# Kernel optimization log

Hardware: AMD Instinct MI355X
Metric: run time of the kernel (lower is better)

## Reference

```python
import jax, jax.numpy as jnp
import numpy as np

D = 8        # q_ndim (= dof_ndim)
HID = 200    # hidden_size
N = 16384    # batch of states
EPS = 0.1    # qdot regularizer coefficient in L()


def _lagrangian(z, Ws, bs):
    # z: (2D,) = [q, qdot]; angular_dims=() so CosSin is an identity pass-through
    v = z[D:]
    h = z
    for W, b in zip(Ws[:-1], bs[:-1]):
        h = jax.nn.softplus(h @ W + b)   # FCsoftplus blocks
    L = (h @ Ws[-1] + bs[-1])[0]          # final Linear -> scalar (Reshape(-1))
    return L + EPS * jnp.dot(v, v)


def setup_inputs():
    key = jax.random.key(0)
    ks = jax.random.split(key, 5)
    z = jax.random.normal(ks[0], (N, 2 * D), dtype=jnp.float32)
    t = jnp.zeros((), dtype=jnp.float32)

    def lin(k, fi, fo, scale):
        return (jax.random.normal(k, (fi, fo), dtype=jnp.float32)
                * jnp.float32(scale / np.sqrt(fi)))

    W0 = lin(ks[1], 2 * D, HID, 1.0)
    W1 = lin(ks[2], HID, HID, 1.0)
    W2 = lin(ks[3], HID, HID, 1.0)
    W3 = lin(ks[4], HID, 1, 0.01)  # small head keeps mass matrix M well conditioned
    b0 = jnp.zeros((HID,), jnp.float32)  # zero_bias init per FCsoftplus/Linear
    b1 = jnp.zeros((HID,), jnp.float32)
    b2 = jnp.zeros((HID,), jnp.float32)
    b3 = jnp.zeros((1,), jnp.float32)
    return dict(t=t, z=z, W0=W0, b0=b0, W1=W1, b1=b1, W2=W2, b2=b2, W3=W3, b3=b3)


def reference(t, z, W0, b0, W1, b1, W2, b2, W3, b3):
    # Euler-Lagrange dynamics (LagrangianDynamics):
    #   M a = dL/dq - (d2L/dq dv) v,  M = d2L/dv2;  dz/dt = [v, a]
    Ws = (W0, W1, W2, W3)
    bs = (b0, b1, b2, b3)
    Lfn = lambda zz: _lagrangian(zz, Ws, bs)

    def dyn_single(zi):
        g = jax.grad(Lfn)(zi)              # (2D,)  = [dL/dq, dL/dv]
        H = jax.jacfwd(jax.grad(Lfn))(zi)  # (2D,2D) Hessian of L wrt z
        v = zi[D:]
        M = H[D:, D:]                      # d(dL/dv)/dv  -> mass matrix
        C = H[D:, :D]                      # d(dL/dv)/dq
        F = g[:D] - C @ v
        a = jnp.linalg.solve(M, F)
        return jnp.concatenate([v, a])     # (2D,)

    return jax.vmap(dyn_single)(z)         # (N, 2D)
```

## Files before the change

kernel.cpp:

```cpp
#include <hip/hip_runtime.h>
#include <math.h>

#define DD 8
#define ZD 16
#define HID 200
#define EPSL 0.1f
#define BS 16
#define NTHREADS 1024
#define NKC 7
#define NMT 13
#define XSTR 216
#define CSTR 212
#define HSTR 20
#define WSTR 208
#define NTAN 8
#define NT4 4

#define KSC 1024.0f
#define SSC 64.0f
#define INV_K (1.0f/1024.0f)
#define INV_KS (1.0f/65536.0f)

typedef _Float16 half8 __attribute__((ext_vector_type(8)));
typedef _Float16 half4v __attribute__((ext_vector_type(4)));
typedef _Float16 half2v __attribute__((ext_vector_type(2)));
typedef __fp16 fp16x2 __attribute__((ext_vector_type(2)));
typedef float float4v __attribute__((ext_vector_type(4)));

#define S4 (NKC*NMT*64*8)
#define OFF_W1T 0
#define OFF_W2T (S4)
#define OFF_W1  (2*S4)
#define OFF_W2  (3*S4)
#define OFF_W0T (4*S4)
#define OFF_W0  (4*S4 + NMT*64*8)
#define WS_HALFS (4*S4 + NMT*64*8 + NKC*64*8)

__global__ void prep(const float* __restrict__ W0, const float* __restrict__ W1,
                     const float* __restrict__ W2, _Float16* __restrict__ ws)
{
    int idx = blockIdx.x * 256 + threadIdx.x;
    if (idx >= WS_HALFS) return;
    float v = 0.f;
    if (idx < 4*S4) {
        int arr = idx / S4, e = idx % S4;
        int kc = e / (NMT*64*8); int r = e % (NMT*64*8);
        int mt = r / (64*8); r %= 64*8;
        int lane = r / 8, j = r % 8;
        int m = mt*16 + (lane & 15);
        int k = kc*32 + (lane >> 4)*8 + j;
        if (m < HID && k < HID) {
            if      (arr == 0) v = W1[k*HID + m];
            else if (arr == 1) v = W2[k*HID + m];
            else if (arr == 2) v = W1[m*HID + k];
            else               v = W2[m*HID + k];
        }
    } else if (idx < OFF_W0) {
        int e = idx - OFF_W0T;
        int mt = e / (64*8); int r = e % (64*8);
        int lane = r / 8, j = r % 8;
        int m = mt*16 + (lane & 15);
        int k = (lane >> 4)*8 + j;
        if (m < HID && k < ZD) v = W0[k*HID + m];
    } else {
        int e = idx - OFF_W0;
        int kc = e / (64*8); int r = e % (64*8);
        int lane = r / 8, j = r % 8;
        int m = (lane & 15);
        int k = kc*32 + (lane >> 4)*8 + j;
        if (k < HID) v = W0[m*HID + k];
    }
    ws[idx] = (_Float16)v;
}

__device__ __forceinline__ half4v pk4(float4v a) {
    half2v lo = __builtin_bit_cast(half2v, __builtin_amdgcn_cvt_pkrtz(a.x, a.y));
    half2v hi = __builtin_bit_cast(half2v, __builtin_amdgcn_cvt_pkrtz(a.z, a.w));
    return __builtin_shufflevector(lo, hi, 0, 1, 2, 3);
}
__device__ __forceinline__ void sig_sp(float x, float& sp, float& sg) {
    float e = __expf(-fabsf(x));
    float r = 1.0f / (1.0f + e);
    sg = (x >= 0.f) ? r : (1.0f - r);
    sp = fmaxf(x, 0.f) + __logf(1.f + e);
}

template<int NTILES>
__device__ __forceinline__ void run_mv(const half8* __restrict__ Asw,
                                       const _Float16* __restrict__ Xsrc,
                                       int mt0, int mtc, int lane,
                                       float4v acc[2][NTILES])
{
    const int lm = lane & 15, q = lane >> 4;
#pragma unroll
    for (int m = 0; m < 2; ++m)
#pragma unroll
        for (int n = 0; n < NTILES; ++n)
            acc[m][n] = (float4v){0.f, 0.f, 0.f, 0.f};
    for (int kc = 0; kc < NKC; ++kc) {
        half8 a[2];
#pragma unroll
        for (int m = 0; m < 2; ++m)
            if (m < mtc) a[m] = Asw[(kc*NMT + mt0 + m)*64 + lane];
        half8 x[NTILES];
#pragma unroll
        for (int n = 0; n < NTILES; ++n)
            x[n] = *(const half8*)(Xsrc + (n*16 + lm)*XSTR + kc*32 + q*8);
#pragma unroll
        for (int m = 0; m < 2; ++m)
            if (m < mtc)
#pragma unroll
                for (int n = 0; n < NTILES; ++n)
                    acc[m][n] = __builtin_amdgcn_mfma_f32_16x16x32_f16(a[m], x[n], acc[m][n], 0, 0, 0);
    }
}

__global__ void __launch_bounds__(NTHREADS, 4)
lnn_main(const float* __restrict__ z,
         const float* __restrict__ W0, const float* __restrict__ b0,
         const float* __restrict__ b1, const float* __restrict__ b2,
         const float* __restrict__ W3,
         const _Float16* __restrict__ ws,
         float* __restrict__ out)
{
    __shared__ alignas(16) _Float16 Xt[128*XSTR];
    __shared__ alignas(16) _Float16 Xb[128*XSTR];
    __shared__ alignas(16) _Float16 Cf[5][16*CSTR];
    __shared__ alignas(16) _Float16 Xz[16*40];
    __shared__ alignas(16) _Float16 bsh[4*WSTR];
    __shared__ alignas(16) _Float16 w0t[NTAN*WSTR];
    __shared__ alignas(16) float gsh[16*HSTR];
    __shared__ alignas(16) float Hr[128*HSTR];

    const int tid  = threadIdx.x;
    const int wave = tid >> 6;
    const int lane = tid & 63;
    const int lm   = lane & 15;
    const int q    = lane >> 4;
    const int s0   = blockIdx.x * BS;

    const int twm  = wave >> 1;
    const int twn  = wave & 1;
    const int mt0t = (twm < 5) ? twm*2 : (twm + 5);
    const int mtct = (twm < 5) ? 2 : 1;

    const half8* W1Tsw = (const half8*)(ws + OFF_W1T);
    const half8* W2Tsw = (const half8*)(ws + OFF_W2T);
    const half8* W1sw  = (const half8*)(ws + OFF_W1);
    const half8* W2sw  = (const half8*)(ws + OFF_W2);
    const half8* W0Tsw = (const half8*)(ws + OFF_W0T);
    const half8* W0sw  = (const half8*)(ws + OFF_W0);

    if (tid < 256) {
        int s = tid >> 4, k = tid & 15;
        Xz[s*40 + k]      = (_Float16)z[(s0 + s)*ZD + k];
        Xz[s*40 + 16 + k] = (_Float16)0.f;
    }
    for (int idx = tid; idx < 128*16; idx += NTHREADS) {
        int r = idx >> 4, c = 200 + (idx & 15);
        Xt[r*XSTR + c] = (_Float16)0.f;
        Xb[r*XSTR + c] = (_Float16)0.f;
    }
    for (int idx = tid; idx < 4*WSTR; idx += NTHREADS) {
        int l = idx / WSTR, u = idx % WSTR;
        float v = 0.f;
        if (u < HID) {
            if      (l == 0) v = b0[u];
            else if (l == 1) v = b1[u];
            else if (l == 2) v = b2[u];
            else             v = KSC * W3[u];
        }
        bsh[idx] = (_Float16)v;
    }
    for (int idx = tid; idx < NTAN*WSTR; idx += NTHREADS) {
        int t = idx / WSTR, u = idx % WSTR;
        w0t[idx] = (_Float16)((u < HID) ? SSC * W0[(DD + t)*HID + u] : 0.f);
    }
    __syncthreads();

    float4v acc1[2][1];
    const int ubf = wave*16 + q*4;

    if (wave < NMT) {
        acc1[0][0] = (float4v){0.f,0.f,0.f,0.f};
        half8 xz = *(const half8*)(Xz + lm*40 + q*8);
        half8 a = W0Tsw[wave*64 + lane];
        acc1[0][0] = __builtin_amdgcn_mfma_f32_16x16x32_f16(a, xz, acc1[0][0], 0, 0, 0);
        half4v bb = *(const half4v*)(&bsh[0*WSTR + ubf]);
        float h[4], p[4];
#pragma unroll
        for (int r = 0; r < 4; ++r) {
            float av = acc1[0][0][r] + (float)bb[r];
            sig_sp(av, h[r], p[r]);
        }
        *(half4v*)(&Xt[lm*XSTR + ubf])     = pk4((float4v){h[0],h[1],h[2],h[3]});
        *(half4v*)(&Cf[0][lm*CSTR + ubf])  = pk4((float4v){p[0],p[1],p[2],p[3]});
    }
    __syncthreads();

    if (wave < NMT) run_mv<1>(W1Tsw, Xt, wave, 1, lane, acc1);
    __syncthreads();
    if (wave < NMT) {
        half4v bb = *(const half4v*)(&bsh[1*WSTR + ubf]);
        float h[4], p[4];
#pragma unroll
        for (int r = 0; r < 4; ++r) {
            float av = acc1[0][0][r] + (float)bb[r];
            sig_sp(av, h[r], p[r]);
        }
        *(half4v*)(&Xt[lm*XSTR + ubf])    = pk4((float4v){h[0],h[1],h[2],h[3]});
        *(half4v*)(&Cf[1][lm*CSTR + ubf]) = pk4((float4v){p[0],p[1],p[2],p[3]});
    }
    __syncthreads();

    if (wave < NMT) run_mv<1>(W2Tsw, Xt, wave, 1, lane, acc1);
    __syncthreads();
    if (wave < NMT) {
        half4v bb = *(const half4v*)(&bsh[2*WSTR + ubf]);
        half4v w3 = *(const half4v*)(&bsh[3*WSTR + ubf]);
        float d2[4], c2[4];
#pragma unroll
        for (int r = 0; r < 4; ++r) {
            float av = acc1[0][0][r] + (float)bb[r];
            float e = __expf(-fabsf(av));
            float rr = 1.f / (1.f + e);
            float sg = (av >= 0.f) ? rr : (1.f - rr);
            float wk = (float)w3[r];
            d2[r] = wk * sg;
            c2[r] = wk * sg * (1.f - sg);
        }
        *(half4v*)(&Xt[lm*XSTR + ubf])    = pk4((float4v){d2[0],d2[1],d2[2],d2[3]});
        *(half4v*)(&Cf[2][lm*CSTR + ubf]) = pk4((float4v){c2[0],c2[1],c2[2],c2[3]});
    }
    __syncthreads();

    if (wave < NMT) run_mv<1>(W2sw, Xt, wave, 1, lane, acc1);
    __syncthreads();
    if (wave < NMT) {
        half4v p1 = *(const half4v*)(&Cf[1][lm*CSTR + ubf]);
        half4v u1 = pk4(acc1[0][0]);
        half4v one = {(_Float16)1.f,(_Float16)1.f,(_Float16)1.f,(_Float16)1.f};
        *(half4v*)(&Xt[lm*XSTR + ubf])    = u1 * p1;
        *(half4v*)(&Cf[3][lm*CSTR + ubf]) = u1 * (one - p1);
    }
    __syncthreads();

    if (wave < NMT) run_mv<1>(W1sw, Xt, wave, 1, lane, acc1);
    __syncthreads();
    if (wave < NMT) {
        half4v p0 = *(const half4v*)(&Cf[0][lm*CSTR + ubf]);
        half4v u0 = pk4(acc1[0][0]);
        half4v one = {(_Float16)1.f,(_Float16)1.f,(_Float16)1.f,(_Float16)1.f};
        half4v d0 = u0 * p0;
        *(half4v*)(&Xt[lm*XSTR + ubf])    = d0;
        *(half4v*)(&Cf[4][lm*CSTR + ubf]) = d0 * (one - p0);
    }
    __syncthreads();

    if (wave == 0) {
        float4v g = (float4v){0.f,0.f,0.f,0.f};
        for (int kc = 0; kc < NKC; ++kc) {
            half8 a = W0sw[kc*64 + lane];
            half8 x = *(const half8*)(Xt + lm*XSTR + kc*32 + q*8);
            g = __builtin_amdgcn_mfma_f32_16x16x32_f16(a, x, g, 0, 0, 0);
        }
        float4v gv; gv.x = g.x*INV_K; gv.y = g.y*INV_K; gv.z = g.z*INV_K; gv.w = g.w*INV_K;
        *(float4v*)(&gsh[lm*HSTR + q*4]) = gv;
    } else {
        for (int idx = tid - 64; idx < 128*50; idx += NTHREADS - 64) {
            int row = idx / 50, u = (idx % 50)*4;
            int s = row & 15, t = row >> 4;
            half4v p0 = *(const half4v*)(&Cf[0][s*CSTR + u]);
            half4v w0 = *(const half4v*)(&w0t[t*WSTR + u]);
            *(half4v*)(&Xb[row*XSTR + u]) = p0 * w0;
        }
    }
    __syncthreads();

    float4v acc4[2][NT4];

    run_mv<NT4>(W1Tsw, Xb + twn*64*XSTR, mt0t, mtct, lane, acc4);
    __syncthreads();
#pragma unroll
    for (int m = 0; m < 2; ++m)
        if (m < mtct) {
            const int ub = (mt0t + m)*16 + q*4;
            half4v p1 = *(const half4v*)(&Cf[1][lm*CSTR + ub]);
#pragma unroll
            for (int n = 0; n < NT4; ++n) {
                int row = (twn*NT4 + n)*16 + lm;
                *(half4v*)(&Xt[row*XSTR + ub]) = pk4(acc4[m][n]) * p1;
            }
        }
    __syncthreads();

    run_mv<NT4>(W2Tsw, Xt + twn*64*XSTR, mt0t, mtct, lane, acc4);
    __syncthreads();
#pragma unroll
    for (int m = 0; m < 2; ++m)
        if (m < mtct) {
            const int ub = (mt0t + m)*16 + q*4;
            half4v c2 = *(const half4v*)(&Cf[2][lm*CSTR + ub]);
#pragma unroll
            for (int n = 0; n < NT4; ++n) {
                int row = (twn*NT4 + n)*16 + lm;
                *(half4v*)(&Xb[row*XSTR + ub]) = pk4(acc4[m][n]) * c2;
            }
        }
    __syncthreads();

    run_mv<NT4>(W2sw, Xb + twn*64*XSTR, mt0t, mtct, lane, acc4);
    __syncthreads();
#pragma unroll
    for (int m = 0; m < 2; ++m)
        if (m < mtct) {
            const int ub = (mt0t + m)*16 + q*4;
            half4v p1 = *(const half4v*)(&Cf[1][lm*CSTR + ub]);
            half4v c3 = *(const half4v*)(&Cf[3][lm*CSTR + ub]);
#pragma unroll
            for (int n = 0; n < NT4; ++n) {
                int row = (twn*NT4 + n)*16 + lm;
                half4v th1 = *(const half4v*)(&Xt[row*XSTR + ub]);
                *(half4v*)(&Xb[row*XSTR + ub]) = pk4(acc4[m][n]) * p1 + c3 * th1;
            }
        }
    __syncthreads();

    run_mv<NT4>(W1sw, Xb + twn*64*XSTR, mt0t, mtct, lane, acc4);
    __syncthreads();
#pragma unroll
    for (int m = 0; m < 2; ++m)
        if (m < mtct) {
            const int ub = (mt0t + m)*16 + q*4;
            half4v p0 = *(const half4v*)(&Cf[0][lm*CSTR + ub]);
            half4v c4 = *(const half4v*)(&Cf[4][lm*CSTR + ub]);
#pragma unroll
            for (int n = 0; n < NT4; ++n) {
                int row = (twn*NT4 + n)*16 + lm;
                half4v w0 = *(const half4v*)(&w0t[(twn*NT4 + n)*WSTR + ub]);
                *(half4v*)(&Xt[row*XSTR + ub]) = pk4(acc4[m][n]) * p0 + c4 * w0;
            }
        }
    __syncthreads();

    if (wave < 8) {
        float4v hacc = (float4v){0.f,0.f,0.f,0.f};
        for (int kc = 0; kc < NKC; ++kc) {
            half8 a = W0sw[kc*64 + lane];
            half8 x = *(const half8*)(Xt + (wave*16 + lm)*XSTR + kc*32 + q*8);
            hacc = __builtin_amdgcn_mfma_f32_16x16x32_f16(a, x, hacc, 0, 0, 0);
        }
        int row = wave*16 + lm;
        float4v hv;
        hv.x = hacc.x*INV_KS; hv.y = hacc.y*INV_KS;
        hv.z = hacc.z*INV_KS; hv.w = hacc.w*INV_KS;
        *(float4v*)(&Hr[row*HSTR + q*4]) = hv;
    }
    __syncthreads();

    if (tid < BS) {
        const int s = tid;
        float M[DD][DD], F[DD], v[DD], a[DD];
#pragma unroll
        for (int c = 0; c < DD; ++c) v[c] = z[(s0 + s)*ZD + DD + c];
#pragma unroll
        for (int r = 0; r < DD; ++r) {
            float f = gsh[s*HSTR + r];
#pragma unroll
            for (int c = 0; c < DD; ++c) {
                M[r][c] = Hr[(r*16 + s)*HSTR + DD + c] + ((r == c) ? 2.f*EPSL : 0.f);
                f -= Hr[(r*16 + s)*HSTR + c] * v[c];
            }
            F[r] = f;
        }
#pragma unroll
        for (int col = 0; col < DD; ++col) {
            const float inv = 1.f / M[col][col];
#pragma unroll
            for (int r = col + 1; r < DD; ++r) {
                const float fac = M[r][col] * inv;
#pragma unroll
                for (int c = col + 1; c < DD; ++c) M[r][c] -= fac * M[col][c];
                F[r] -= fac * F[col];
            }
        }
#pragma unroll
        for (int r = DD - 1; r >= 0; --r) {
            float ssum = F[r];
#pragma unroll
            for (int c = r + 1; c < DD; ++c) ssum -= M[r][c] * a[c];
            a[r] = ssum / M[r][r];
        }
        float* op = out + (size_t)(s0 + s)*ZD;
#pragma unroll
        for (int c = 0; c < DD; ++c) { op[c] = v[c]; op[DD + c] = a[c]; }
    }
}

extern "C" void kernel_launch(void* const* d_in, const int* in_sizes, int n_in,
                              void* d_out, int out_size, void* d_ws, size_t ws_size,
                              hipStream_t stream)
{
    const float* z  = (const float*)d_in[1];
    const float* W0 = (const float*)d_in[2];
    const float* b0 = (const float*)d_in[3];
    const float* W1 = (const float*)d_in[4];
    const float* b1 = (const float*)d_in[5];
    const float* W2 = (const float*)d_in[6];
    const float* b2 = (const float*)d_in[7];
    const float* W3 = (const float*)d_in[8];
    float* out = (float*)d_out;
    _Float16* ws = (_Float16*)d_ws;

    const int n = in_sizes[1] / (2*DD);

    prep<<<dim3((WS_HALFS + 255)/256), dim3(256), 0, stream>>>(W0, W1, W2, ws);
    lnn_main<<<dim3(n / BS), dim3(NTHREADS), 0, stream>>>(
        z, W0, b0, b1, b2, W3, ws, out);
}
```

Before: 160.1 us.

## Overlap forward/backward matvecs with tangent pass and fuse tangent input construction

Restructures the kernel schedule so the single-row forward and backward matvecs (into a new FB buffer) run in the same barrier phases as the 128-row tangent matmuls. The first tangent matmul now builds its input p0*w0 in registers instead of staging it through shared memory, and the gradient head runs on wave 13 alongside the last tangent step. The aim is fewer __syncthreads phases and less idle time for waves. All shared arrays are packed into one buffer with explicit offsets and padding. The cost is higher register pressure from keeping acc4 and acc1 live together, plus extra zero-padding setup.

```diff
diff --git a/kernel.cpp b/kernel.cpp
--- a/kernel.cpp
+++ b/kernel.cpp
@@ -10,10 +10,9 @@
 #define NKC 7
 #define NMT 13
 #define XSTR 216
-#define CSTR 212
+#define CSTR 216
+#define WSTR 208
 #define HSTR 20
-#define WSTR 208
-#define NTAN 8
 #define NT4 4
 
 #define KSC 1024.0f
@@ -24,7 +23,6 @@
 typedef _Float16 half8 __attribute__((ext_vector_type(8)));
 typedef _Float16 half4v __attribute__((ext_vector_type(4)));
 typedef _Float16 half2v __attribute__((ext_vector_type(2)));
-typedef __fp16 fp16x2 __attribute__((ext_vector_type(2)));
 typedef float float4v __attribute__((ext_vector_type(4)));
 
 #define S4 (NKC*NMT*64*8)
@@ -35,6 +33,17 @@
 #define OFF_W0T (4*S4)
 #define OFF_W0  (4*S4 + NMT*64*8)
 #define WS_HALFS (4*S4 + NMT*64*8 + NKC*64*8)
+
+#define CFSZ  (16*CSTR)
+#define O_XT  0
+#define O_XB  (128*XSTR + 8)
+#define O_CF  (O_XB + 128*XSTR)
+#define O_BSH (O_CF + 5*CFSZ)
+#define O_W0T (O_BSH + 4*WSTR)
+#define O_XZ  (O_W0T + 8*WSTR + 24)
+#define O_GSH (O_XZ + 16*40)
+#define O_HR  (O_GSH + 256)
+#define SMEM_HALFS (O_HR + 128*HSTR*2)
 
 __global__ void prep(const float* __restrict__ W0, const float* __restrict__ W1,
                      const float* __restrict__ W2, _Float16* __restrict__ ws)
@@ -123,14 +132,16 @@
          const _Float16* __restrict__ ws,
          float* __restrict__ out)
 {
-    __shared__ alignas(16) _Float16 Xt[128*XSTR];
-    __shared__ alignas(16) _Float16 Xb[128*XSTR];
-    __shared__ alignas(16) _Float16 Cf[5][16*CSTR];
-    __shared__ alignas(16) _Float16 Xz[16*40];
-    __shared__ alignas(16) _Float16 bsh[4*WSTR];
-    __shared__ alignas(16) _Float16 w0t[NTAN*WSTR];
-    __shared__ alignas(16) float gsh[16*HSTR];
-    __shared__ alignas(16) float Hr[128*HSTR];
+    __shared__ alignas(16) _Float16 smem[SMEM_HALFS];
+    _Float16* const Xt  = smem + O_XT;
+    _Float16* const Xb  = smem + O_XB;
+    _Float16* const Cf  = smem + O_CF;
+    _Float16* const bsh = smem + O_BSH;
+    _Float16* const w0t = smem + O_W0T;
+    _Float16* const Xz  = smem + O_XZ;
+    float*    const gsh = (float*)(smem + O_GSH);
+    float*    const Hr  = (float*)(smem + O_HR);
+    _Float16* const FB  = smem + O_HR;
 
     const int tid  = threadIdx.x;
     const int wave = tid >> 6;
@@ -160,6 +171,18 @@
         int r = idx >> 4, c = 200 + (idx & 15);
         Xt[r*XSTR + c] = (_Float16)0.f;
         Xb[r*XSTR + c] = (_Float16)0.f;
+    }
+    for (int idx = tid; idx < 16*16; idx += NTHREADS) {
+        int r = idx >> 4, c = 200 + (idx & 15);
+        FB[r*XSTR + c] = (_Float16)0.f;
+    }
+    if (tid < 8) {
+        Xt[128*XSTR + tid] = (_Float16)0.f;
+        FB[16*XSTR + tid]  = (_Float16)0.f;
+    }
+    for (int idx = tid; idx < 5*16*8; idx += NTHREADS) {
+        int j = idx >> 7, r = (idx >> 3) & 15, c = 208 + (idx & 7);
+        Cf[j*CFSZ + r*CSTR + c] = (_Float16)0.f;
     }
     for (int idx = tid; idx < 4*WSTR; idx += NTHREADS) {
         int l = idx / WSTR, u = idx % WSTR;
@@ -172,20 +195,21 @@
         }
         bsh[idx] = (_Float16)v;
     }
-    for (int idx = tid; idx < NTAN*WSTR; idx += NTHREADS) {
+    for (int idx = tid; idx < 8*WSTR + 24; idx += NTHREADS) {
         int t = idx / WSTR, u = idx % WSTR;
-        w0t[idx] = (_Float16)((u < HID) ? SSC * W0[(DD + t)*HID + u] : 0.f);
+        w0t[idx] = (_Float16)((t < 8 && u < HID) ? SSC * W0[(DD + t)*HID + u] : 0.f);
     }
     __syncthreads();
 
     float4v acc1[2][1];
+    float4v acc4[2][NT4];
     const int ubf = wave*16 + q*4;
 
     if (wave < NMT) {
         acc1[0][0] = (float4v){0.f,0.f,0.f,0.f};
         half8 xz = *(const half8*)(Xz + lm*40 + q*8);
-        half8 a = W0Tsw[wave*64 + lane];
-        acc1[0][0] = __builtin_amdgcn_mfma_f32_16x16x32_f16(a, xz, acc1[0][0], 0, 0, 0);
+        half8 aw = W0Tsw[wave*64 + lane];
+        acc1[0][0] = __builtin_amdgcn_mfma_f32_16x16x32_f16(aw, xz, acc1[0][0], 0, 0, 0);
         half4v bb = *(const half4v*)(&bsh[0*WSTR + ubf]);
         float h[4], p[4];
 #pragma unroll
@@ -193,12 +217,12 @@
             float av = acc1[0][0][r] + (float)bb[r];
             sig_sp(av, h[r], p[r]);
         }
-        *(half4v*)(&Xt[lm*XSTR + ubf])     = pk4((float4v){h[0],h[1],h[2],h[3]});
-        *(half4v*)(&Cf[0][lm*CSTR + ubf])  = pk4((float4v){p[0],p[1],p[2],p[3]});
-    }
-    __syncthreads();
-
-    if (wave < NMT) run_mv<1>(W1Tsw, Xt, wave, 1, lane, acc1);
+        *(half4v*)(&FB[lm*XSTR + ubf])          = pk4((float4v){h[0],h[1],h[2],h[3]});
+        *(half4v*)(&Cf[0*CFSZ + lm*CSTR + ubf]) = pk4((float4v){p[0],p[1],p[2],p[3]});
+    }
+    __syncthreads();
+
+    if (wave < NMT) run_mv<1>(W1Tsw, FB, wave, 1, lane, acc1);
     __syncthreads();
     if (wave < NMT) {
         half4v bb = *(const half4v*)(&bsh[1*WSTR + ubf]);
@@ -208,13 +232,50 @@
             float av = acc1[0][0][r] + (float)bb[r];
             sig_sp(av, h[r], p[r]);
         }
-        *(half4v*)(&Xt[lm*XSTR + ubf])    = pk4((float4v){h[0],h[1],h[2],h[3]});
-        *(half4v*)(&Cf[1][lm*CSTR + ubf]) = pk4((float4v){p[0],p[1],p[2],p[3]});
-    }
-    __syncthreads();
-
-    if (wave < NMT) run_mv<1>(W2Tsw, Xt, wave, 1, lane, acc1);
-    __syncthreads();
+        *(half4v*)(&FB[lm*XSTR + ubf])          = pk4((float4v){h[0],h[1],h[2],h[3]});
+        *(half4v*)(&Cf[1*CFSZ + lm*CSTR + ubf]) = pk4((float4v){p[0],p[1],p[2],p[3]});
+    }
+    __syncthreads();
+
+    {
+#pragma unroll
+        for (int m = 0; m < 2; ++m)
+#pragma unroll
+            for (int n = 0; n < NT4; ++n)
+                acc4[m][n] = (float4v){0.f, 0.f, 0.f, 0.f};
+        for (int kc = 0; kc < NKC; ++kc) {
+            half8 a[2];
+#pragma unroll
+            for (int m = 0; m < 2; ++m)
+                if (m < mtct) a[m] = W1Tsw[(kc*NMT + mt0t + m)*64 + lane];
+            half8 p0 = *(const half8*)(Cf + 0*CFSZ + lm*CSTR + kc*32 + q*8);
+            half8 x[NT4];
+#pragma unroll
+            for (int n = 0; n < NT4; ++n) {
+                half8 w0 = *(const half8*)(w0t + (twn*NT4 + n)*WSTR + kc*32 + q*8);
+                x[n] = p0 * w0;
+            }
+#pragma unroll
+            for (int m = 0; m < 2; ++m)
+                if (m < mtct)
+#pragma unroll
+                    for (int n = 0; n < NT4; ++n)
+                        acc4[m][n] = __builtin_amdgcn_mfma_f32_16x16x32_f16(a[m], x[n], acc4[m][n], 0, 0, 0);
+        }
+        if (wave < NMT) run_mv<1>(W2Tsw, FB, wave, 1, lane, acc1);
+    }
+    __syncthreads();
+#pragma unroll
+    for (int m = 0; m < 2; ++m)
+        if (m < mtct) {
+            const int ub = (mt0t + m)*16 + q*4;
+            half4v p1 = *(const half4v*)(&Cf[1*CFSZ + lm*CSTR + ub]);
+#pragma unroll
+            for (int n = 0; n < NT4; ++n) {
+                int row = (twn*NT4 + n)*16 + lm;
+                *(half4v*)(&Xt[row*XSTR + ub]) = pk4(acc4[m][n]) * p1;
+            }
+        }
     if (wave < NMT) {
         half4v bb = *(const half4v*)(&bsh[2*WSTR + ubf]);
         half4v w3 = *(const half4v*)(&bsh[3*WSTR + ubf]);
@@ -229,94 +290,43 @@
             d2[r] = wk * sg;
             c2[r] = wk * sg * (1.f - sg);
         }
-        *(half4v*)(&Xt[lm*XSTR + ubf])    = pk4((float4v){d2[0],d2[1],d2[2],d2[3]});
-        *(half4v*)(&Cf[2][lm*CSTR + ubf]) = pk4((float4v){c2[0],c2[1],c2[2],c2[3]});
-    }
-    __syncthreads();
-
-    if (wave < NMT) run_mv<1>(W2sw, Xt, wave, 1, lane, acc1);
-    __syncthreads();
-    if (wave < NMT) {
-        half4v p1 = *(const half4v*)(&Cf[1][lm*CSTR + ubf]);
-        half4v u1 = pk4(acc1[0][0]);
-        half4v one = {(_Float16)1.f,(_Float16)1.f,(_Float16)1.f,(_Float16)1.f};
-        *(half4v*)(&Xt[lm*XSTR + ubf])    = u1 * p1;
-        *(half4v*)(&Cf[3][lm*CSTR + ubf]) = u1 * (one - p1);
-    }
-    __syncthreads();
-
-    if (wave < NMT) run_mv<1>(W1sw, Xt, wave, 1, lane, acc1);
-    __syncthreads();
-    if (wave < NMT) {
-        half4v p0 = *(const half4v*)(&Cf[0][lm*CSTR + ubf]);
-        half4v u0 = pk4(acc1[0][0]);
-        half4v one = {(_Float16)1.f,(_Float16)1.f,(_Float16)1.f,(_Float16)1.f};
-        half4v d0 = u0 * p0;
-        *(half4v*)(&Xt[lm*XSTR + ubf])    = d0;
-        *(half4v*)(&Cf[4][lm*CSTR + ubf]) = d0 * (one - p0);
-    }
-    __syncthreads();
-
-    if (wave == 0) {
-        float4v g = (float4v){0.f,0.f,0.f,0.f};
-        for (int kc = 0; kc < NKC; ++kc) {
-            half8 a = W0sw[kc*64 + lane];
-            half8 x = *(const half8*)(Xt + lm*XSTR + kc*32 + q*8);
-            g = __builtin_amdgcn_mfma_f32_16x16x32_f16(a, x, g, 0, 0, 0);
-        }
-        float4v gv; gv.x = g.x*INV_K; gv.y = g.y*INV_K; gv.z = g.z*INV_K; gv.w = g.w*INV_K;
-        *(float4v*)(&gsh[lm*HSTR + q*4]) = gv;
-    } else {
-        for (int idx = tid - 64; idx < 128*50; idx += NTHREADS - 64) {
-            int row = idx / 50, u = (idx % 50)*4;
-            int s = row & 15, t = row >> 4;
-            half4v p0 = *(const half4v*)(&Cf[0][s*CSTR + u]);
-            half4v w0 = *(const half4v*)(&w0t[t*WSTR + u]);
-            *(half4v*)(&Xb[row*XSTR + u]) = p0 * w0;
-        }
-    }
-    __syncthreads();
-
-    float4v acc4[2][NT4];
-
-    run_mv<NT4>(W1Tsw, Xb + twn*64*XSTR, mt0t, mtct, lane, acc4);
+        *(half4v*)(&FB[lm*XSTR + ubf])          = pk4((float4v){d2[0],d2[1],d2[2],d2[3]});
+        *(half4v*)(&Cf[2*CFSZ + lm*CSTR + ubf]) = pk4((float4v){c2[0],c2[1],c2[2],c2[3]});
+    }
+    __syncthreads();
+
+    run_mv<NT4>(W2Tsw, Xt + twn*64*XSTR, mt0t, mtct, lane, acc4);
+    if (wave < NMT) run_mv<1>(W2sw, FB, wave, 1, lane, acc1);
     __syncthreads();
 #pragma unroll
     for (int m = 0; m < 2; ++m)
         if (m < mtct) {
             const int ub = (mt0t + m)*16 + q*4;
-            half4v p1 = *(const half4v*)(&Cf[1][lm*CSTR + ub]);
+            half4v c2 = *(const half4v*)(&Cf[2*CFSZ + lm*CSTR + ub]);
 #pragma unroll
             for (int n = 0; n < NT4; ++n) {
                 int row = (twn*NT4 + n)*16 + lm;
-                *(half4v*)(&Xt[row*XSTR + ub]) = pk4(acc4[m][n]) * p1;
-            }
-        }
-    __syncthreads();
-
-    run_mv<NT4>(W2Tsw, Xt + twn*64*XSTR, mt0t, mtct, lane, acc4);
+                *(half4v*)(&Xb[row*XSTR + ub]) = pk4(acc4[m][n]) * c2;
+            }
+        }
+    if (wave < NMT) {
+        half4v p1 = *(const half4v*)(&Cf[1*CFSZ + lm*CSTR + ubf]);
+        half4v u1 = pk4(acc1[0][0]);
+        half4v one = {(_Float16)1.f,(_Float16)1.f,(_Float16)1.f,(_Float16)1.f};
+        *(half4v*)(&FB[lm*XSTR + ubf])          = u1 * p1;
+        *(half4v*)(&Cf[3*CFSZ + lm*CSTR + ubf]) = u1 * (one - p1);
+    }
+    __syncthreads();
+
+    run_mv<NT4>(W2sw, Xb + twn*64*XSTR, mt0t, mtct, lane, acc4);
+    if (wave < NMT) run_mv<1>(W1sw, FB, wave, 1, lane, acc1);
     __syncthreads();
 #pragma unroll
     for (int m = 0; m < 2; ++m)
         if (m < mtct) {
             const int ub = (mt0t + m)*16 + q*4;
-            half4v c2 = *(const half4v*)(&Cf[2][lm*CSTR + ub]);
-#pragma unroll
-            for (int n = 0; n < NT4; ++n) {
-                int row = (twn*NT4 + n)*16 + lm;
-                *(half4v*)(&Xb[row*XSTR + ub]) = pk4(acc4[m][n]) * c2;
-            }
-        }
-    __syncthreads();
-
-    run_mv<NT4>(W2sw, Xb + twn*64*XSTR, mt0t, mtct, lane, acc4);
-    __syncthreads();
-#pragma unroll
-    for (int m = 0; m < 2; ++m)
-        if (m < mtct) {
-            const int ub = (mt0t + m)*16 + q*4;
-            half4v p1 = *(const half4v*)(&Cf[1][lm*CSTR + ub]);
-            half4v c3 = *(const half4v*)(&Cf[3][lm*CSTR + ub]);
+            half4v p1 = *(const half4v*)(&Cf[1*CFSZ + lm*CSTR + ub]);
+            half4v c3 = *(const half4v*)(&Cf[3*CFSZ + lm*CSTR + ub]);
 #pragma unroll
             for (int n = 0; n < NT4; ++n) {
                 int row = (twn*NT4 + n)*16 + lm;
@@ -324,16 +334,36 @@
                 *(half4v*)(&Xb[row*XSTR + ub]) = pk4(acc4[m][n]) * p1 + c3 * th1;
             }
         }
+    if (wave < NMT) {
+        half4v p0 = *(const half4v*)(&Cf[0*CFSZ + lm*CSTR + ubf]);
+        half4v u0 = pk4(acc1[0][0]);
+        half4v one = {(_Float16)1.f,(_Float16)1.f,(_Float16)1.f,(_Float16)1.f};
+        half4v d0 = u0 * p0;
+        *(half4v*)(&FB[lm*XSTR + ubf])          = d0;
+        *(half4v*)(&Cf[4*CFSZ + lm*CSTR + ubf]) = d0 * (one - p0);
+    }
     __syncthreads();
 
     run_mv<NT4>(W1sw, Xb + twn*64*XSTR, mt0t, mtct, lane, acc4);
-    __syncthreads();
+    if (wave == 13) {
+        float4v g = (float4v){0.f,0.f,0.f,0.f};
+        for (int kc = 0; kc < NKC; ++kc) {
+            half8 a = W0sw[kc*64 + lane];
+            half8 x = *(const half8*)(FB + lm*XSTR + kc*32 + q*8);
+            g = __builtin_amdgcn_mfma_f32_16x16x32_f16(a, x, g, 0, 0, 0);
+        }
+        if (q < 2) {
+            float4v gv;
+            gv.x = g.x*INV_K; gv.y = g.y*INV_K; gv.z = g.z*INV_K; gv.w = g.w*INV_K;
+            *(float4v*)(&gsh[lm*8 + q*4]) = gv;
+        }
+    }
 #pragma unroll
     for (int m = 0; m < 2; ++m)
         if (m < mtct) {
             const int ub = (mt0t + m)*16 + q*4;
-            half4v p0 = *(const half4v*)(&Cf[0][lm*CSTR + ub]);
-            half4v c4 = *(const half4v*)(&Cf[4][lm*CSTR + ub]);
+            half4v p0 = *(const half4v*)(&Cf[0*CFSZ + lm*CSTR + ub]);
+            half4v c4 = *(const half4v*)(&Cf[4*CFSZ + lm*CSTR + ub]);
 #pragma unroll
             for (int n = 0; n < NT4; ++n) {
                 int row = (twn*NT4 + n)*16 + lm;
@@ -365,7 +395,7 @@
         for (int c = 0; c < DD; ++c) v[c] = z[(s0 + s)*ZD + DD + c];
 #pragma unroll
         for (int r = 0; r < DD; ++r) {
-            float f = gsh[s*HSTR + r];
+            float f = gsh[s*8 + r];
 #pragma unroll
             for (int c = 0; c < DD; ++c) {
                 M[r][c] = Hr[(r*16 + s)*HSTR + DD + c] + ((r == c) ? 2.f*EPSL : 0.f);
```

Measured after the change: 156.6 us. -2.2%, faster.
